# Kernel optimization log

Hardware: AMD Instinct MI355X
Metric: run time of the kernel (lower is better)

Reference implementation:

```python
import jax, jax.numpy as jnp
import numpy as np

B, S, D_IN = 16, 1024, 1024
H, D_OUT = 16, 128

def setup_inputs() -> dict:
    key = jax.random.key(0)
    k1, k2, k3 = jax.random.split(key, 3)
    x = jax.random.normal(k1, (B, S, D_IN), dtype=jnp.float32)
    W = jax.random.normal(k2, (H, 3, D_IN, D_OUT), dtype=jnp.float32) * (1.0 / np.sqrt(D_IN))
    Wo = jax.random.normal(k3, (H * D_OUT, D_OUT), dtype=jnp.float32) * (1.0 / np.sqrt(H * D_OUT))
    return {"x": x, "W": W, "Wo": Wo}

def reference(x, W, Wo):
    # x: [B,S,D_IN], W: [H,3,D_IN,E], Wo: [H*E,E]
    E = W.shape[-1]
    q = jnp.einsum('bsd,hde->bhse', x, W[:, 0])
    k = jnp.einsum('bsd,hde->bhse', x, W[:, 1])
    v = jnp.einsum('bsd,hde->bhse', x, W[:, 2])
    # NOTE: source divides by (output_dim * 0.5), not sqrt(output_dim)
    scores = jnp.einsum('bhse,bhte->bhst', q, k) / (E * 0.5)
    attn = jax.nn.softmax(scores, axis=-1)
    o = jnp.einsum('bhst,bhte->bhse', attn, v)          # [B,H,S,E]
    o = jnp.transpose(o, (0, 2, 1, 3)).reshape(x.shape[0], x.shape[1], -1)  # concat heads
    return jnp.einsum('bsf,fe->bse', o, Wo)
```

## Files before the change

kernel.cpp:

```cpp
#include <hip/hip_runtime.h>

typedef unsigned short u16;
typedef _Float16 f16;
typedef __attribute__((ext_vector_type(8))) _Float16 half8;
typedef __attribute__((ext_vector_type(8))) short short8;
typedef __attribute__((ext_vector_type(4))) float f32x4;
typedef __attribute__((ext_vector_type(4))) float f4;
typedef __attribute__((ext_vector_type(4))) u16 u16x4;

#define B_ 16
#define S_ 1024
#define DIN_ 1024
#define H_ 16
#define E_ 128

#define EXPK 0.0225546041776533f

__device__ __forceinline__ u16 f2h(float f) {
  f16 h = (f16)f;
  return __builtin_bit_cast(u16, h);
}

__device__ __forceinline__ void gl2lds16(const u16* g, u16* l) {
  __builtin_amdgcn_global_load_lds((const __attribute__((address_space(1))) void*)g,
                                   (__attribute__((address_space(3))) void*)l, 16, 0, 0);
}

__global__ __launch_bounds__(256) void zero_f32(float* __restrict__ p) {
  int i = (blockIdx.x * 256 + threadIdx.x) * 4;
  f4 z = {0.f, 0.f, 0.f, 0.f};
  *reinterpret_cast<f4*>(p + i) = z;
}

__global__ __launch_bounds__(256) void cvt_f32_f16(const float* __restrict__ in,
                                                   u16* __restrict__ out) {
  int i = (blockIdx.x * 256 + threadIdx.x) * 4;
  f4 v = *reinterpret_cast<const f4*>(in + i);
  u16x4 o;
  o[0] = f2h(v[0]); o[1] = f2h(v[1]); o[2] = f2h(v[2]); o[3] = f2h(v[3]);
  *reinterpret_cast<u16x4*>(out + i) = o;
}

__global__ __launch_bounds__(256) void transpose_cvt(const float* __restrict__ in,
                                                     u16* __restrict__ out,
                                                     int R, int C) {
  __shared__ float tile[32][33];
  const size_t moff = (size_t)blockIdx.z * R * C;
  const float* src = in + moff;
  u16* dst = out + moff;
  int c0 = blockIdx.x * 32, r0 = blockIdx.y * 32;
  int tx = threadIdx.x & 31, ty = threadIdx.x >> 5;
#pragma unroll
  for (int i = 0; i < 32; i += 8)
    tile[ty + i][tx] = src[(size_t)(r0 + ty + i) * C + c0 + tx];
  __syncthreads();
#pragma unroll
  for (int i = 0; i < 32; i += 8)
    dst[(size_t)(c0 + ty + i) * R + r0 + tx] = f2h(tile[tx][ty + i]);
}

template<int MODE, int KSPLIT, int K>
__global__ __launch_bounds__(256) void gemm_bt(const u16* __restrict__ A,
                                               const u16* __restrict__ BT,
                                               u16* __restrict__ q, u16* __restrict__ kk,
                                               u16* __restrict__ vT, float* __restrict__ out) {
  const int tid = threadIdx.x;
  const int m0 = blockIdx.x * 128;
  const u16* Bblk = BT + (size_t)blockIdx.y * 128 * K;
  __shared__ __align__(16) u16 smem[132 * 128];
  u16* As = smem;
  u16* Bs = smem + 8192;
  const int w = tid >> 6, lane = tid & 63;
  const int quad = lane >> 4, ln = lane & 15;
  const int wr = w >> 1, wc = w & 1;

  const int kbeg = (KSPLIT > 1) ? blockIdx.z * (K / KSPLIT) : 0;
  constexpr int KLEN = K / KSPLIT;

  const int rr = lane >> 3;
  const int cc = (lane & 7) ^ rr;
  const u16* agp[4];
  const u16* bgp[4];
#pragma unroll
  for (int i = 0; i < 4; i++) {
    int row = i * 32 + w * 8 + rr;
    agp[i] = A + (size_t)(m0 + row) * K + kbeg + cc * 8;
    bgp[i] = Bblk + (size_t)row * K + kbeg + cc * 8;
  }

  int offA[4][2], offB[4][2];
#pragma unroll
  for (int mt = 0; mt < 4; mt++) {
    int row = wr * 64 + mt * 16 + ln;
#pragma unroll
    for (int k2 = 0; k2 < 2; k2++)
      offA[mt][k2] = row * 64 + (((k2 * 4 + quad) ^ (ln & 7)) * 8);
  }
#pragma unroll
  for (int nt = 0; nt < 4; nt++) {
    int row = wc * 64 + nt * 16 + ln;
#pragma unroll
    for (int k2 = 0; k2 < 2; k2++)
      offB[nt][k2] = row * 64 + (((k2 * 4 + quad) ^ (ln & 7)) * 8);
  }

  f32x4 acc[4][4];
  f32x4 zero = {0.f, 0.f, 0.f, 0.f};
#pragma unroll
  for (int mt = 0; mt < 4; mt++)
#pragma unroll
    for (int nt = 0; nt < 4; nt++) acc[mt][nt] = zero;

#pragma unroll
  for (int k0 = 0; k0 < KLEN; k0 += 64) {
    __syncthreads();
#pragma unroll
    for (int i = 0; i < 4; i++) {
      gl2lds16(agp[i] + k0, As + i * 2048 + w * 512);
      gl2lds16(bgp[i] + k0, Bs + i * 2048 + w * 512);
    }
    __syncthreads();
#pragma unroll
    for (int k2 = 0; k2 < 2; k2++) {
      half8 af[4], bfr[4];
#pragma unroll
      for (int mt = 0; mt < 4; mt++)
        af[mt] = *reinterpret_cast<const half8*>(&As[offA[mt][k2]]);
#pragma unroll
      for (int nt = 0; nt < 4; nt++)
        bfr[nt] = *reinterpret_cast<const half8*>(&Bs[offB[nt][k2]]);
#pragma unroll
      for (int mt = 0; mt < 4; mt++)
#pragma unroll
        for (int nt = 0; nt < 4; nt++)
          acc[mt][nt] = __builtin_amdgcn_mfma_f32_16x16x32_f16(af[mt], bfr[nt], acc[mt][nt], 0, 0, 0);
    }
  }

  if (MODE == 0) {
    const int h = blockIdx.y / 3, c = blockIdx.y % 3;
    if (c < 2) {
      u16* dst = (c == 0) ? q : kk;
      const float sc = (c == 0) ? EXPK : 1.0f;
#pragma unroll
      for (int mt = 0; mt < 4; mt++)
#pragma unroll
        for (int nt = 0; nt < 4; nt++)
#pragma unroll
          for (int r = 0; r < 4; r++) {
            int row = wr * 64 + mt * 16 + quad * 4 + r;
            int tok = m0 + row;
            int bb = tok >> 10, s = tok & 1023;
            int e = wc * 64 + nt * 16 + ln;
            dst[(((size_t)bb * H_ + h) * S_ + s) * E_ + e] = f2h(acc[mt][nt][r] * sc);
          }
    } else {
      __syncthreads();
#pragma unroll
      for (int mt = 0; mt < 4; mt++)
#pragma unroll
        for (int nt = 0; nt < 4; nt++)
#pragma unroll
          for (int r = 0; r < 4; r++) {
            int row = wr * 64 + mt * 16 + quad * 4 + r;
            int e = wc * 64 + nt * 16 + ln;
            int srow = (row & 0x60) | ((row & 12) << 1) | ((row & 16) >> 2) | (row & 3);
            smem[e * 132 + srow] = f2h(acc[mt][nt][r]);
          }
      __syncthreads();
      const int bb = m0 >> 10, sbase = m0 & 1023;
      u16* vbase = vT + (((size_t)bb * H_ + h) * E_) * S_;
#pragma unroll
      for (int i = 0; i < 8; i++) {
        int e = (tid >> 4) + i * 16, s0 = (tid & 15) * 8;
        *reinterpret_cast<short8*>(&vbase[(size_t)e * S_ + sbase + s0]) =
            *reinterpret_cast<const short8*>(&smem[e * 132 + s0]);
      }
    }
  } else {
#pragma unroll
    for (int mt = 0; mt < 4; mt++)
#pragma unroll
      for (int nt = 0; nt < 4; nt++)
#pragma unroll
        for (int r = 0; r < 4; r++) {
          int row = wr * 64 + mt * 16 + quad * 4 + r;
          int e = wc * 64 + nt * 16 + ln;
          if (KSPLIT > 1)
            atomicAdd(&out[(size_t)(m0 + row) * E_ + e], acc[mt][nt][r]);
          else
            out[(size_t)(m0 + row) * E_ + e] = acc[mt][nt][r];
        }
  }
}

struct SmemKV {
  u16 ks[64 * 128];
  u16 vs[128 * 64];
};
union SmemAttn {
  u16 qs[128 * 132];
  SmemKV s;
};

__global__ __launch_bounds__(256, 3) void attn_kernel(const u16* __restrict__ qg,
                                                      const u16* __restrict__ kg,
                                                      const u16* __restrict__ vg,
                                                      u16* __restrict__ og) {
  __shared__ __align__(16) SmemAttn sm;
  const int tid = threadIdx.x;
  const int id = blockIdx.x;
  const int g = id >> 6, qt = (id >> 3) & 7, x = id & 7;
  const int hb = g * 8 + x;
  const int b = hb >> 4, h = hb & 15;
  const int q0 = qt * 128;
  const size_t bh = (size_t)(b * H_ + h);
  const u16* qp = qg + bh * S_ * E_;
  const u16* kp = kg + bh * S_ * E_;
  const u16* vp = vg + bh * E_ * S_;
  const int w = tid >> 6, lane = tid & 63, quad = lane >> 4, ln = lane & 15;

#pragma unroll
  for (int i = 0; i < 8; i++) {
    int idx = tid + i * 256;
    int row = idx >> 4, col = (idx & 15) * 8;
    *reinterpret_cast<short8*>(&sm.qs[row * 132 + col]) =
        *reinterpret_cast<const short8*>(&qp[(size_t)(q0 + row) * E_ + col]);
  }
  __syncthreads();
  half8 qf[2][4];
#pragma unroll
  for (int mt = 0; mt < 2; mt++)
#pragma unroll
    for (int ks = 0; ks < 4; ks++)
      qf[mt][ks] = *reinterpret_cast<const half8*>(
          &sm.qs[(w * 32 + mt * 16 + ln) * 132 + ks * 32 + quad * 8]);

  const int krow = w * 4 + (lane >> 4);
  const int kc = ((lane & 15) & 8) | (((lane & 15) & 7) ^ (krow & 7));
  const u16* kbase = kp + (size_t)krow * E_ + kc * 8;
  const int vrow = w * 8 + (lane >> 3);
  const int vc = (lane & 7) ^ ((lane >> 3) & 7);
  const u16* vbase = vp + (size_t)vrow * S_ + vc * 8;

  f32x4 zero = {0.f, 0.f, 0.f, 0.f};
  f32x4 oa[2][8];
#pragma unroll
  for (int mt = 0; mt < 2; mt++)
#pragma unroll
    for (int nt = 0; nt < 8; nt++) oa[mt][nt] = zero;
  float lsum[2] = {0.f, 0.f};

  for (int kt = 0; kt < 16; kt++) {
    __syncthreads();
#pragma unroll
    for (int i = 0; i < 4; i++) {
      gl2lds16(kbase + (size_t)kt * 8192 + i * 16 * E_, &sm.s.ks[(i * 256 + w * 64) * 8]);
      gl2lds16(vbase + (size_t)kt * 64 + i * 32 * S_,   &sm.s.vs[(i * 256 + w * 64) * 8]);
    }
    __syncthreads();

    f32x4 sa[2][4];
#pragma unroll
    for (int mt = 0; mt < 2; mt++)
#pragma unroll
      for (int nt = 0; nt < 4; nt++) sa[mt][nt] = zero;
#pragma unroll
    for (int ks = 0; ks < 4; ks++) {
      half8 kf[4];
#pragma unroll
      for (int nt = 0; nt < 4; nt++) {
        int c = ks * 4 + quad;
        int cs = (c & 8) | ((c & 7) ^ (ln & 7));
        kf[nt] = *reinterpret_cast<const half8*>(&sm.s.ks[(nt * 16 + ln) * 128 + cs * 8]);
      }
#pragma unroll
      for (int mt = 0; mt < 2; mt++)
#pragma unroll
        for (int nt = 0; nt < 4; nt++)
          sa[mt][nt] = __builtin_amdgcn_mfma_f32_16x16x32_f16(kf[nt], qf[mt][ks], sa[mt][nt], 0, 0, 0);
    }

    half8 pfr[2][2];
#pragma unroll
    for (int mt = 0; mt < 2; mt++) {
      float psum = 0.f;
#pragma unroll
      for (int k2 = 0; k2 < 2; k2++) {
        half8 ph;
#pragma unroll
        for (int hhalf = 0; hhalf < 2; hhalf++)
#pragma unroll
          for (int r = 0; r < 4; r++) {
            float p = exp2f(sa[mt][k2 * 2 + hhalf][r]);
            psum += p;
            ph[hhalf * 4 + r] = (f16)p;
          }
        pfr[mt][k2] = ph;
      }
      lsum[mt] += psum;
    }

#pragma unroll
    for (int k2 = 0; k2 < 2; k2++) {
#pragma unroll
      for (int nt8 = 0; nt8 < 8; nt8++) {
        int c = k2 * 4 + quad;
        int cs = c ^ (ln & 7);
        half8 vf = *reinterpret_cast<const half8*>(&sm.s.vs[(nt8 * 16 + ln) * 64 + cs * 8]);
#pragma unroll
        for (int mt = 0; mt < 2; mt++)
          oa[mt][nt8] = __builtin_amdgcn_mfma_f32_16x16x32_f16(pfr[mt][k2], vf, oa[mt][nt8], 0, 0, 0);
      }
    }
  }

#pragma unroll
  for (int mt = 0; mt < 2; mt++) {
    float l = lsum[mt];
    l += __shfl_xor(l, 16);
    l += __shfl_xor(l, 32);
#pragma unroll
    for (int r = 0; r < 4; r++) {
      float lr = __shfl(l, quad * 4 + r);
      float rl = 1.0f / lr;
      int srow = q0 + w * 32 + mt * 16 + quad * 4 + r;
      size_t base = ((size_t)b * S_ + srow) * (H_ * E_) + (size_t)h * E_;
#pragma unroll
      for (int nt8 = 0; nt8 < 8; nt8++)
        og[base + nt8 * 16 + ln] = f2h(oa[mt][nt8][r] * rl);
    }
  }
}

extern "C" void kernel_launch(void* const* d_in, const int* in_sizes, int n_in,
                              void* d_out, int out_size, void* d_ws, size_t ws_size,
                              hipStream_t stream) {
  const float* x = (const float*)d_in[0];
  const float* W = (const float*)d_in[1];
  const float* Wo = (const float*)d_in[2];
  float* out = (float*)d_out;
  char* ws = (char*)d_ws;

  const size_t WBT_BYTES = (size_t)H_ * 3 * DIN_ * E_ * 2;
  const size_t WOT_BYTES = (size_t)H_ * E_ * E_ * 2 * 2;
  const size_t FIXED = WBT_BYTES + WOT_BYTES;

  const size_t XB_PER   = (size_t)S_ * DIN_ * 2;
  const size_t QKV_PER  = (size_t)H_ * S_ * E_ * 2;
  const size_t OB_PER   = (size_t)S_ * H_ * E_ * 2;
  const size_t PER_ITEM = XB_PER + 3 * QKV_PER + OB_PER;

  int Bc = 1;
  for (int c = 16; c >= 1; c >>= 1) {
    if (FIXED + (size_t)c * PER_ITEM <= ws_size) { Bc = c; break; }
  }

  u16* WbT = (u16*)(ws);
  u16* WoT = (u16*)(ws + WBT_BYTES);
  char* cb = ws + FIXED;
  u16* xb  = (u16*)(cb);
  u16* qb  = (u16*)(cb + (size_t)Bc * XB_PER);
  u16* kb  = (u16*)(cb + (size_t)Bc * (XB_PER + QKV_PER));
  u16* vTb = (u16*)(cb + (size_t)Bc * (XB_PER + 2 * QKV_PER));
  u16* ob  = (u16*)(cb + (size_t)Bc * (XB_PER + 3 * QKV_PER));

  zero_f32<<<out_size / 1024, 256, 0, stream>>>(out);
  transpose_cvt<<<dim3(4, 32, 48), 256, 0, stream>>>(W, WbT, DIN_, E_);
  transpose_cvt<<<dim3(4, 64, 1), 256, 0, stream>>>(Wo, WoT, H_ * E_, E_);

  for (int b0 = 0; b0 < B_; b0 += Bc) {
    const float* xc = x + (size_t)b0 * S_ * DIN_;
    cvt_f32_f16<<<Bc * S_ * DIN_ / 1024, 256, 0, stream>>>(xc, xb);
    gemm_bt<0, 1, DIN_><<<dim3(Bc * 8, 48), 256, 0, stream>>>(xb, WbT, qb, kb, vTb, nullptr);
    attn_kernel<<<Bc * 128, 256, 0, stream>>>(qb, kb, vTb, ob);
    gemm_bt<1, 4, H_ * E_><<<dim3(Bc * 8, 1, 4), 256, 0, stream>>>(ob, WoT, nullptr, nullptr,
                                                                   nullptr, out + (size_t)b0 * S_ * E_);
  }
}
```

Before: 556.0 us.

## Use 256x256 tiled QKV projection GEMM with 512 threads and double buffering

Replaces the 128x128-tile QKV projection GEMM with a new kernel that computes 256x256 output tiles using 8 waves and double-buffered LDS staging via direct global-to-LDS loads. It also raises MFMA scheduling priority. Larger tiles raise arithmetic intensity and cut redundant global reads of x and W. The epilogue now handles tiles that span two q/k/v slabs and writes V transposed through LDS. The cost is 128KB of LDS per block and many accumulator registers, which limits occupancy to one block per CU.

```diff
diff --git a/kernel.cpp b/kernel.cpp
--- a/kernel.cpp
+++ b/kernel.cpp
@@ -57,6 +57,140 @@
 #pragma unroll
   for (int i = 0; i < 32; i += 8)
     dst[(size_t)(c0 + ty + i) * R + r0 + tx] = f2h(tile[tx][ty + i]);
+}
+
+template<int K>
+__global__ __launch_bounds__(512) void gemm256_qkv(const u16* __restrict__ A,
+                                                   const u16* __restrict__ BT,
+                                                   u16* __restrict__ q, u16* __restrict__ kk,
+                                                   u16* __restrict__ vT) {
+  constexpr int KT = K / 64;
+  const int tid = threadIdx.x;
+  const int m0 = blockIdx.x * 256;
+  const int nt0 = blockIdx.y;
+  const u16* Bblk = BT + (size_t)nt0 * 256 * K;
+  __shared__ __align__(16) u16 smem[65536];
+  const int w = tid >> 6, lane = tid & 63;
+  const int quad = lane >> 4, ln = lane & 15;
+  const int wr = w >> 2, wc = w & 3;
+
+  const int srow = tid >> 3;
+  const int scc = (tid & 7) ^ (srow & 7);
+  const u16* agp = A + (size_t)(m0 + srow) * K + scc * 8;
+  const u16* bgp = Bblk + (size_t)srow * K + scc * 8;
+
+#define STAGE256(buf, t)                                                     \
+  do {                                                                       \
+    u16* ab_ = smem + (buf) * 32768;                                         \
+    _Pragma("unroll") for (int i_ = 0; i_ < 4; i_++) {                       \
+      gl2lds16(agp + (t) * 64 + (size_t)i_ * 64 * K, ab_ + i_ * 4096 + tid * 8);        \
+      gl2lds16(bgp + (t) * 64 + (size_t)i_ * 64 * K, ab_ + 16384 + i_ * 4096 + tid * 8);\
+    }                                                                        \
+  } while (0)
+
+  int offA[8][2], offB[4][2];
+#pragma unroll
+  for (int mt = 0; mt < 8; mt++) {
+    int row = wr * 128 + mt * 16 + ln;
+#pragma unroll
+    for (int k2 = 0; k2 < 2; k2++)
+      offA[mt][k2] = row * 64 + (((k2 * 4 + quad) ^ (ln & 7)) * 8);
+  }
+#pragma unroll
+  for (int nt = 0; nt < 4; nt++) {
+    int row = wc * 64 + nt * 16 + ln;
+#pragma unroll
+    for (int k2 = 0; k2 < 2; k2++)
+      offB[nt][k2] = 16384 + row * 64 + (((k2 * 4 + quad) ^ (ln & 7)) * 8);
+  }
+
+  f32x4 acc[8][4];
+  f32x4 zero = {0.f, 0.f, 0.f, 0.f};
+#pragma unroll
+  for (int mt = 0; mt < 8; mt++)
+#pragma unroll
+    for (int nt = 0; nt < 4; nt++) acc[mt][nt] = zero;
+
+  STAGE256(0, 0);
+#pragma unroll
+  for (int t = 0; t < KT; t++) {
+    asm volatile("s_waitcnt vmcnt(0)" ::: "memory");
+    asm volatile("s_barrier" ::: "memory");
+    if (t < KT - 1) STAGE256((t + 1) & 1, t + 1);
+    const u16* ab = smem + (t & 1) * 32768;
+#pragma unroll
+    for (int qd = 0; qd < 4; qd++) {
+      const int mh = qd >> 1, nh = qd & 1;
+      half8 af[4][2], bf[2][2];
+#pragma unroll
+      for (int k2 = 0; k2 < 2; k2++) {
+#pragma unroll
+        for (int i = 0; i < 4; i++)
+          af[i][k2] = *reinterpret_cast<const half8*>(&ab[offA[mh * 4 + i][k2]]);
+#pragma unroll
+        for (int j = 0; j < 2; j++)
+          bf[j][k2] = *reinterpret_cast<const half8*>(&ab[offB[nh * 2 + j][k2]]);
+      }
+      __builtin_amdgcn_s_setprio(1);
+#pragma unroll
+      for (int k2 = 0; k2 < 2; k2++)
+#pragma unroll
+        for (int i = 0; i < 4; i++)
+#pragma unroll
+          for (int j = 0; j < 2; j++)
+            acc[mh * 4 + i][nh * 2 + j] = __builtin_amdgcn_mfma_f32_16x16x32_f16(
+                af[i][k2], bf[j][k2], acc[mh * 4 + i][nh * 2 + j], 0, 0, 0);
+      __builtin_amdgcn_s_setprio(0);
+    }
+  }
+#undef STAGE256
+
+  __syncthreads();
+  const int slab = nt0 * 2 + (wc >> 1);
+  const int h = slab / 3, c = slab % 3;
+  if (c < 2) {
+    u16* dst = (c == 0) ? q : kk;
+    const float sc = (c == 0) ? EXPK : 1.0f;
+#pragma unroll
+    for (int mt = 0; mt < 8; mt++)
+#pragma unroll
+      for (int nt = 0; nt < 4; nt++)
+#pragma unroll
+        for (int r = 0; r < 4; r++) {
+          int tok = m0 + wr * 128 + mt * 16 + quad * 4 + r;
+          int bb = tok >> 10, s = tok & 1023;
+          int e = (wc & 1) * 64 + nt * 16 + ln;
+          dst[(((size_t)bb * H_ + h) * S_ + s) * E_ + e] = f2h(acc[mt][nt][r] * sc);
+        }
+  } else {
+#pragma unroll
+    for (int mt = 0; mt < 8; mt++)
+#pragma unroll
+      for (int nt = 0; nt < 4; nt++) {
+        int tok0 = wr * 128 + mt * 16 + quad * 4;
+        int ptok0 = (tok0 & ~31) | ((tok0 & 12) << 1) | ((tok0 & 16) >> 2);
+        int e = (wc & 1) * 64 + nt * 16 + ln;
+        u16x4 pp;
+#pragma unroll
+        for (int r = 0; r < 4; r++) pp[r] = f2h(acc[mt][nt][r]);
+        *reinterpret_cast<u16x4*>(&smem[e * 260 + ptok0]) = pp;
+      }
+  }
+  __syncthreads();
+  int vslab = -1;
+  if ((nt0 * 2) % 3 == 2) vslab = 0;
+  else if ((nt0 * 2 + 1) % 3 == 2) vslab = 1;
+  if (vslab >= 0) {
+    const int hv = (nt0 * 2 + vslab) / 3;
+    const int bb = m0 >> 10, sbase = m0 & 1023;
+    u16* vbase = vT + (((size_t)bb * H_ + hv) * E_) * S_;
+#pragma unroll
+    for (int i = 0; i < 8; i++) {
+      int e = (tid >> 5) + i * 16, s0 = (tid & 31) * 8;
+      *reinterpret_cast<short8*>(&vbase[(size_t)e * S_ + sbase + s0]) =
+          *reinterpret_cast<const short8*>(&smem[e * 260 + s0]);
+    }
+  }
 }
 
 template<int MODE, int KSPLIT, int K>
@@ -137,47 +271,7 @@
     }
   }
 
-  if (MODE == 0) {
-    const int h = blockIdx.y / 3, c = blockIdx.y % 3;
-    if (c < 2) {
-      u16* dst = (c == 0) ? q : kk;
-      const float sc = (c == 0) ? EXPK : 1.0f;
-#pragma unroll
-      for (int mt = 0; mt < 4; mt++)
-#pragma unroll
-        for (int nt = 0; nt < 4; nt++)
-#pragma unroll
-          for (int r = 0; r < 4; r++) {
-            int row = wr * 64 + mt * 16 + quad * 4 + r;
-            int tok = m0 + row;
-            int bb = tok >> 10, s = tok & 1023;
-            int e = wc * 64 + nt * 16 + ln;
-            dst[(((size_t)bb * H_ + h) * S_ + s) * E_ + e] = f2h(acc[mt][nt][r] * sc);
-          }
-    } else {
-      __syncthreads();
-#pragma unroll
-      for (int mt = 0; mt < 4; mt++)
-#pragma unroll
-        for (int nt = 0; nt < 4; nt++)
-#pragma unroll
-          for (int r = 0; r < 4; r++) {
-            int row = wr * 64 + mt * 16 + quad * 4 + r;
-            int e = wc * 64 + nt * 16 + ln;
-            int srow = (row & 0x60) | ((row & 12) << 1) | ((row & 16) >> 2) | (row & 3);
-            smem[e * 132 + srow] = f2h(acc[mt][nt][r]);
-          }
-      __syncthreads();
-      const int bb = m0 >> 10, sbase = m0 & 1023;
-      u16* vbase = vT + (((size_t)bb * H_ + h) * E_) * S_;
-#pragma unroll
-      for (int i = 0; i < 8; i++) {
-        int e = (tid >> 4) + i * 16, s0 = (tid & 15) * 8;
-        *reinterpret_cast<short8*>(&vbase[(size_t)e * S_ + sbase + s0]) =
-            *reinterpret_cast<const short8*>(&smem[e * 132 + s0]);
-      }
-    }
-  } else {
+  {
 #pragma unroll
     for (int mt = 0; mt < 4; mt++)
 #pragma unroll
@@ -372,7 +466,7 @@
   for (int b0 = 0; b0 < B_; b0 += Bc) {
     const float* xc = x + (size_t)b0 * S_ * DIN_;
     cvt_f32_f16<<<Bc * S_ * DIN_ / 1024, 256, 0, stream>>>(xc, xb);
-    gemm_bt<0, 1, DIN_><<<dim3(Bc * 8, 48), 256, 0, stream>>>(xb, WbT, qb, kb, vTb, nullptr);
+    gemm256_qkv<DIN_><<<dim3(Bc * 4, 24), 512, 0, stream>>>(xb, WbT, qb, kb, vTb);
     attn_kernel<<<Bc * 128, 256, 0, stream>>>(qb, kb, vTb, ob);
     gemm_bt<1, 4, H_ * E_><<<dim3(Bc * 8, 1, 4), 256, 0, stream>>>(ob, WoT, nullptr, nullptr,
                                                                    nullptr, out + (size_t)b0 * S_ * E_);
```

After: 555.8 us. No clear change (-0.0%).
